# Kernel tuning notes

Measured on AMD Instinct MI355X. Metric: run time of the kernel, lower is better.

Reference implementation:

```python
import jax, jax.numpy as jnp
import numpy as np

VOCAB, POS = 50000, 64
WDIM, PDIM = 256, 64
LSTM_H = 512          # total bidirectional width
H = LSTM_H // 2       # per-direction hidden
MLP = 512
SEQ = 512


def _lstm_dir(x, Wih, Whh, bih, bhh, reverse):
    # x: [T, in]; Wih: [4H, in]; Whh: [4H, H]; gate order i,f,g,o (PyTorch)
    Hd = Whh.shape[1]
    def step(carry, xt):
        h, c = carry
        g = xt @ Wih.T + bih + h @ Whh.T + bhh
        i, f, gg, o = jnp.split(g, 4, axis=-1)
        c = jax.nn.sigmoid(f) * c + jax.nn.sigmoid(i) * jnp.tanh(gg)
        h = jax.nn.sigmoid(o) * jnp.tanh(c)
        return (h, c), h
    xs = x[::-1] if reverse else x
    init = (jnp.zeros((Hd,), x.dtype), jnp.zeros((Hd,), x.dtype))
    _, hs = jax.lax.scan(step, init, xs)
    return hs[::-1] if reverse else hs


def _bilstm_layer(x, Wih, Whh, bih, bhh):
    # params stacked over direction: [2, ...]
    hf = _lstm_dir(x, Wih[0], Whh[0], bih[0], bhh[0], False)
    hb = _lstm_dir(x, Wih[1], Whh[1], bih[1], bhh[1], True)
    return jnp.concatenate([hf, hb], axis=-1)  # [T, 2H]


def setup_inputs() -> dict:
    key = jax.random.key(0)
    ks = jax.random.split(key, 16)
    s = 0.05
    inp = {
        "word_tensor": jax.random.randint(ks[0], (SEQ,), 0, VOCAB),
        "pos_tensor": jax.random.randint(ks[1], (SEQ,), 0, POS),
        "word_emb": jax.random.normal(ks[2], (VOCAB, WDIM), jnp.float32) * s,
        "pos_emb": jax.random.normal(ks[3], (POS, PDIM), jnp.float32) * s,
        # layer 0: input = WDIM+PDIM = 320
        "wih0": jax.random.normal(ks[4], (2, 4 * H, WDIM + PDIM), jnp.float32) * s,
        "whh0": jax.random.normal(ks[5], (2, 4 * H, H), jnp.float32) * s,
        "bih0": jax.random.normal(ks[6], (2, 4 * H), jnp.float32) * s,
        "bhh0": jax.random.normal(ks[7], (2, 4 * H), jnp.float32) * s,
        # layer 1: input = 2H = LSTM_H
        "wih1": jax.random.normal(ks[8], (2, 4 * H, LSTM_H), jnp.float32) * s,
        "whh1": jax.random.normal(ks[9], (2, 4 * H, H), jnp.float32) * s,
        "bih1": jax.random.normal(ks[10], (2, 4 * H), jnp.float32) * s,
        "bhh1": jax.random.normal(ks[11], (2, 4 * H), jnp.float32) * s,
        # pairwise MLP: Linear(2*LSTM_H -> MLP), output_layer(MLP -> 1)
        "W_lin": jax.random.normal(ks[12], (MLP, 2 * LSTM_H), jnp.float32) * s,
        "b_lin": jax.random.normal(ks[13], (MLP,), jnp.float32) * s,
        "w_out": jax.random.normal(ks[14], (1, MLP), jnp.float32) * s,
        "b_out": jax.random.normal(ks[15], (1,), jnp.float32) * s,
    }
    return inp


def reference(word_tensor, pos_tensor, word_emb, pos_emb,
              wih0, whh0, bih0, bhh0, wih1, whh1, bih1, bhh1,
              W_lin, b_lin, w_out, b_out):
    # embeddings: [T, 320]
    embeds = jnp.concatenate([word_emb[word_tensor], pos_emb[pos_tensor]], axis=-1)
    x = _bilstm_layer(embeds, wih0, whh0, bih0, bhh0)
    lstm_out = _bilstm_layer(x, wih1, whh1, bih1, bhh1)  # [T, LSTM_H]
    # Fused pairwise scoring: Linear(cat(h_h, h_m)) = h_h @ W1.T + h_m @ W2.T + b
    W1, W2 = W_lin[:, :LSTM_H], W_lin[:, LSTM_H:]
    u = lstm_out @ W1.T  # [T, MLP] head half
    v = lstm_out @ W2.T  # [T, MLP] modifier half
    neuron = jnp.tanh(u[:, None, :] + v[None, :, :] + b_lin)  # [T, T, MLP]
    score = neuron @ w_out[0] + b_out[0]                      # [T, T]
    n = score.shape[0]
    # original puts NaN on the diagonal (invalid h==m pairs); use 0.0 sentinel
    return jnp.where(jnp.eye(n, dtype=bool), 0.0, score)
```

## Files before the change

kernel.cpp:

```cpp
#include <hip/hip_runtime.h>
#include <cstddef>
#include <cstdint>

constexpr int kSeq = 512;
constexpr int kH   = 256;
constexpr int kG   = 1024;
constexpr int kE   = 320;
constexpr int kLH  = 512;
constexpr int kMLP = 512;

typedef _Float16 h2 __attribute__((ext_vector_type(2)));

__device__ __forceinline__ float fexp2f(float x) {
  float r; asm("v_exp_f32 %0, %1" : "=v"(r) : "v"(x)); return r;
}
__device__ __forceinline__ float frcpf(float x) {
  float r; asm("v_rcp_f32 %0, %1" : "=v"(r) : "v"(x)); return r;
}
__device__ __forceinline__ float sigm(float x) {
  return frcpf(1.0f + fexp2f(-1.4426950408889634f * x));
}
__device__ __forceinline__ float tanh_(float x) {
  return 1.0f - 2.0f * frcpf(1.0f + fexp2f(2.8853900817779268f * x));
}

__device__ __forceinline__ float fdot2(unsigned int w, unsigned int h, float c) {
#if __has_builtin(__builtin_amdgcn_fdot2)
  return __builtin_amdgcn_fdot2(__builtin_bit_cast(h2, w),
                                __builtin_bit_cast(h2, h), c, false);
#else
  const h2 wv = __builtin_bit_cast(h2, w);
  const h2 hv = __builtin_bit_cast(h2, h);
  return c + (float)wv.x * (float)hv.x + (float)wv.y * (float)hv.y;
#endif
}

__device__ __forceinline__ unsigned int packh2(float a, float b) {
  h2 v; v.x = (_Float16)a; v.y = (_Float16)b;
  return __builtin_bit_cast(unsigned int, v);
}

__global__ void embed_k(const int* __restrict__ wt, const int* __restrict__ pt,
                        const float* __restrict__ we, const float* __restrict__ pe,
                        float* __restrict__ X) {
  const int t = blockIdx.x;
  const int c = threadIdx.x;
  const int w = wt[t];
  const int p = pt[t];
  X[t * kE + c] = (c < 256) ? we[(size_t)w * 256 + c] : pe[p * 64 + (c - 256)];
}

__global__ __launch_bounds__(256) void pack_wh_k(
    const float* __restrict__ whh0, const float* __restrict__ whh1,
    unsigned int* __restrict__ wh16) {
  const int idx = blockIdx.x * 256 + threadIdx.x;
  const int layer = idx >> 18;
  const int li = idx & 262143;
  const int rowg = li >> 7;
  const int c2 = li & 127;
  const float* src = (layer ? whh1 : whh0) + (size_t)rowg * kH + c2 * 2;
  wh16[idx] = packh2(src[0], src[1]);
}

template <int BM, int BN, int BK>
__global__ __launch_bounds__(256) void gemm_nt(
    const float* __restrict__ A, int lda,
    const float* __restrict__ B, int ldb,
    const float* __restrict__ b1, const float* __restrict__ b2, float scale,
    float* __restrict__ C, int csm, int csn, int K) {
  const int tid = threadIdx.x;
  const int m0 = blockIdx.y * BM;
  const int n0 = blockIdx.x * BN;
  __shared__ float As[BK][BM];
  __shared__ float Bs[BK][BN];
  const int lm = tid >> 2;
  const int lk = tid & 3;
  const int tx = tid & 15;
  const int ty = tid >> 4;
  float acc[4][4] = {};
  for (int k0 = 0; k0 < K; k0 += BK) {
    const float4 av = *(const float4*)(A + (size_t)(m0 + lm) * lda + k0 + lk * 4);
    const float4 bv = *(const float4*)(B + (size_t)(n0 + lm) * ldb + k0 + lk * 4);
    __syncthreads();
    As[lk * 4 + 0][lm] = av.x; As[lk * 4 + 1][lm] = av.y;
    As[lk * 4 + 2][lm] = av.z; As[lk * 4 + 3][lm] = av.w;
    Bs[lk * 4 + 0][lm] = bv.x; Bs[lk * 4 + 1][lm] = bv.y;
    Bs[lk * 4 + 2][lm] = bv.z; Bs[lk * 4 + 3][lm] = bv.w;
    __syncthreads();
#pragma unroll
    for (int kk = 0; kk < BK; ++kk) {
      const float4 a = *(const float4*)&As[kk][ty * 4];
      const float4 b = *(const float4*)&Bs[kk][tx * 4];
      acc[0][0] = fmaf(a.x, b.x, acc[0][0]);
      acc[0][1] = fmaf(a.x, b.y, acc[0][1]);
      acc[0][2] = fmaf(a.x, b.z, acc[0][2]);
      acc[0][3] = fmaf(a.x, b.w, acc[0][3]);
      acc[1][0] = fmaf(a.y, b.x, acc[1][0]);
      acc[1][1] = fmaf(a.y, b.y, acc[1][1]);
      acc[1][2] = fmaf(a.y, b.z, acc[1][2]);
      acc[1][3] = fmaf(a.y, b.w, acc[1][3]);
      acc[2][0] = fmaf(a.z, b.x, acc[2][0]);
      acc[2][1] = fmaf(a.z, b.y, acc[2][1]);
      acc[2][2] = fmaf(a.z, b.z, acc[2][2]);
      acc[2][3] = fmaf(a.z, b.w, acc[2][3]);
      acc[3][0] = fmaf(a.w, b.x, acc[3][0]);
      acc[3][1] = fmaf(a.w, b.y, acc[3][1]);
      acc[3][2] = fmaf(a.w, b.z, acc[3][2]);
      acc[3][3] = fmaf(a.w, b.w, acc[3][3]);
    }
  }
#pragma unroll
  for (int ii = 0; ii < 4; ++ii) {
#pragma unroll
    for (int jj = 0; jj < 4; ++jj) {
      const int m = m0 + ty * 4 + ii;
      const int n = n0 + tx * 4 + jj;
      float v = acc[ii][jj];
      if (b1) v += b1[n];
      if (b2) v += b2[n];
      C[(size_t)m * csm + (size_t)n * csn] = v * scale;
    }
  }
}

__global__ __launch_bounds__(1024)
__attribute__((amdgpu_waves_per_eu(4, 4)))
void lstm_scan_2cu(
    const unsigned int* __restrict__ wh16,
    const float* __restrict__ pre,
    float* __restrict__ out,
    float* __restrict__ comm)
{
  const int d = blockIdx.x >> 1;
  const int s = blockIdx.x & 1;
  const int t = threadIdx.x;
  const int w = t >> 6;
  const int L = t & 63;
  const int ch = w & 1;
  const int r  = (w >> 1) * 64 + L;
  const int g  = r >> 7;
  const int j  = r & 127;
  const int grow = g * kH + s * 128 + j;
  const bool early = (ch == s);

  uint4 wr[16];
  {
    const uint4* wp = (const uint4*)wh16 + ((size_t)d * kG + grow) * 32 + ch * 16;
#pragma unroll
    for (int k = 0; k < 16; ++k) wr[k] = wp[k];
  }

  __shared__ __align__(16) _Float16 hh16[kH];
  __shared__ float pbuf[512];
  __shared__ float gbuf[512];
  if (t < 128) ((h2*)hh16)[t] = h2{(_Float16)0.f, (_Float16)0.f};
  float c = 0.0f;
  __syncthreads();

  const uint4* hh4 = (const uint4*)hh16;
  float* cm = comm + (size_t)d * kSeq * kH;

  const bool isPoller = early && ((w >> 1) < 2);
  const int pe = (w >> 1) * 64 + L;
  const int re = (1 - s) * 128 + pe;

  for (int u = 0; u < kSeq; ++u) {
    const int ts = d ? (kSeq - 1 - u) : u;
    float pg = 0.0f;
    if (!early) pg = pre[((size_t)d * kSeq + ts) * kG + grow];

    if (early) {
      const uint4* hp = hh4 + ch * 16;
      float a0 = 0.f, a1 = 0.f, a2 = 0.f, a3 = 0.f;
#pragma unroll
      for (int k = 0; k < 16; ++k) {
        const uint4 hv = hp[k];
        a0 = fdot2(wr[k].x, hv.x, a0);
        a1 = fdot2(wr[k].y, hv.y, a1);
        a2 = fdot2(wr[k].z, hv.z, a2);
        a3 = fdot2(wr[k].w, hv.w, a3);
      }
      pbuf[r] = (a0 + a1) + (a2 + a3);
      if (isPoller && u > 0) {
        const float* src = &cm[(size_t)(u - 1) * kH + re];
        float a = __hip_atomic_load(src, __ATOMIC_RELAXED, __HIP_MEMORY_SCOPE_AGENT);
        float b = __hip_atomic_load(src, __ATOMIC_RELAXED, __HIP_MEMORY_SCOPE_AGENT);
        while (a == 0.0f) {
          a = b;
          b = __hip_atomic_load(src, __ATOMIC_RELAXED, __HIP_MEMORY_SCOPE_AGENT);
        }
        hh16[re] = (_Float16)(a - 2.0f);
      }
    }
    __syncthreads();

    if (!early) {
      const uint4* hp = hh4 + ch * 16;
      float a0 = 0.f, a1 = 0.f, a2 = 0.f, a3 = 0.f;
#pragma unroll
      for (int k = 0; k < 16; ++k) {
        const uint4 hv = hp[k];
        a0 = fdot2(wr[k].x, hv.x, a0);
        a1 = fdot2(wr[k].y, hv.y, a1);
        a2 = fdot2(wr[k].z, hv.z, a2);
        a3 = fdot2(wr[k].w, hv.w, a3);
      }
      gbuf[r] = pbuf[r] + (a0 + a1) + (a2 + a3) + pg;
    }
    __syncthreads();

    if (t < 128) {
      const float gi = gbuf[t];
      const float gf = gbuf[128 + t];
      const float gg = gbuf[256 + t];
      const float go = gbuf[384 + t];
      const float iv = sigm(gi), fv = sigm(gf);
      const float gv = tanh_(gg), ov = sigm(go);
      c = fv * c + iv * gv;
      const float h = ov * tanh_(c);
      const int e = s * 128 + t;
      __hip_atomic_store(&cm[(size_t)u * kH + e], h + 2.0f,
                         __ATOMIC_RELAXED, __HIP_MEMORY_SCOPE_AGENT);
      hh16[e] = (_Float16)h;
      out[(size_t)ts * kLH + d * kH + e] = h;
    }
    __syncthreads();
  }
}

__global__ __launch_bounds__(512) void score_k(
    const float* __restrict__ Up, const float* __restrict__ VT,
    const float* __restrict__ wout, const float* __restrict__ bout,
    float* __restrict__ out) {
  const int i = blockIdx.x;
  const int j = threadIdx.x;
  __shared__ float u_sh[kMLP];
  __shared__ float w_sh[kMLP];
  u_sh[j] = Up[(size_t)i * kMLP + j];
  w_sh[j] = wout[j];
  __syncthreads();
  float acc = 0.0f;
#pragma unroll 4
  for (int m = 0; m < kMLP; ++m) {
    const float x = u_sh[m] + VT[(size_t)m * kSeq + j];
    const float th = 1.0f - 2.0f * frcpf(1.0f + fexp2f(x));
    acc = fmaf(th, w_sh[m], acc);
  }
  const float s = acc + bout[0];
  out[(size_t)i * kSeq + j] = (j == i) ? 0.0f : s;
}

extern "C" void kernel_launch(void* const* d_in, const int* in_sizes, int n_in,
                              void* d_out, int out_size, void* d_ws, size_t ws_size,
                              hipStream_t stream) {
  const int*   wt   = (const int*)d_in[0];
  const int*   pt   = (const int*)d_in[1];
  const float* wemb = (const float*)d_in[2];
  const float* pemb = (const float*)d_in[3];
  const float* wih0 = (const float*)d_in[4];
  const float* whh0 = (const float*)d_in[5];
  const float* bih0 = (const float*)d_in[6];
  const float* bhh0 = (const float*)d_in[7];
  const float* wih1 = (const float*)d_in[8];
  const float* whh1 = (const float*)d_in[9];
  const float* bih1 = (const float*)d_in[10];
  const float* bhh1 = (const float*)d_in[11];
  const float* wlin = (const float*)d_in[12];
  const float* blin = (const float*)d_in[13];
  const float* wout = (const float*)d_in[14];
  const float* bout = (const float*)d_in[15];
  float* outp = (float*)d_out;

  float* ws   = (float*)d_ws;
  float* X    = ws;
  float* PG0  = X + kSeq * kE;
  float* X1   = PG0 + 2 * kSeq * kG;
  float* PG1  = X1 + kSeq * kLH;
  float* LOUT = PG1 + 2 * kSeq * kG;
  float* U    = LOUT + kSeq * kLH;
  float* VT   = U + kSeq * kMLP;
  float* COMM0 = VT + kSeq * kMLP;
  float* COMM1 = COMM0 + 2 * kSeq * kH;
  unsigned int* WH16 = (unsigned int*)(COMM1 + 2 * kSeq * kH);

  const float SC = 2.8853900817779268f;

  hipMemsetAsync(COMM0, 0, 2 * 2 * kSeq * kH * sizeof(float), stream);

  embed_k<<<kSeq, kE, 0, stream>>>(wt, pt, wemb, pemb, X);
  pack_wh_k<<<2048, 256, 0, stream>>>(whh0, whh1, WH16);

  for (int d = 0; d < 2; ++d) {
    gemm_nt<64, 64, 16><<<dim3(kG / 64, kSeq / 64), 256, 0, stream>>>(
        X, kE, wih0 + (size_t)d * kG * kE, kE,
        bih0 + d * kG, bhh0 + d * kG, 1.0f,
        PG0 + (size_t)d * kSeq * kG, kG, 1, kE);
  }
  lstm_scan_2cu<<<4, 1024, 0, stream>>>(WH16, PG0, X1, COMM0);

  for (int d = 0; d < 2; ++d) {
    gemm_nt<64, 64, 16><<<dim3(kG / 64, kSeq / 64), 256, 0, stream>>>(
        X1, kLH, wih1 + (size_t)d * kG * kLH, kLH,
        bih1 + d * kG, bhh1 + d * kG, 1.0f,
        PG1 + (size_t)d * kSeq * kG, kG, 1, kLH);
  }
  lstm_scan_2cu<<<4, 1024, 0, stream>>>(WH16 + 2 * kG * 128, PG1, LOUT, COMM1);

  gemm_nt<64, 64, 16><<<dim3(kMLP / 64, kSeq / 64), 256, 0, stream>>>(
      LOUT, kLH, wlin, 2 * kLH, nullptr, nullptr, SC,
      U, kMLP, 1, kLH);
  gemm_nt<64, 64, 16><<<dim3(kMLP / 64, kSeq / 64), 256, 0, stream>>>(
      LOUT, kLH, wlin + kLH, 2 * kLH, blin, nullptr, SC,
      VT, 1, kSeq, kLH);

  score_k<<<kSeq, 512, 0, stream>>>(U, VT, wout, bout, outp);
}
```

Measured before the change: 1.940 ms.

## Restructure 2-CU LSTM step to two barriers with dedicated poller wave

Before, each recurrent step ran an early half-dot product that overlapped with polling for the peer CU's h, then a late half, then the gate stage, separated by three barriers. Now both halves of the dot product run together into a double pbuf. Gate threads add the partial sums plus the preactivation loads, and a separate group of waves polls the peer's h for the current step in the same phase. This drops one barrier per step. The cost is that the peer-h wait now sits on the critical path just before the next step's barrier, rather than overlapping with half of the matvec.

```diff
diff --git a/kernel.cpp b/kernel.cpp
--- a/kernel.cpp
+++ b/kernel.cpp
@@ -141,7 +141,6 @@
   const int g  = r >> 7;
   const int j  = r & 127;
   const int grow = g * kH + s * 128 + j;
-  const bool early = (ch == s);
 
   uint4 wr[16];
   {
@@ -151,25 +150,25 @@
   }
 
   __shared__ __align__(16) _Float16 hh16[kH];
-  __shared__ float pbuf[512];
-  __shared__ float gbuf[512];
+  __shared__ float pbuf[2][512];
   if (t < 128) ((h2*)hh16)[t] = h2{(_Float16)0.f, (_Float16)0.f};
   float c = 0.0f;
   __syncthreads();
 
   const uint4* hh4 = (const uint4*)hh16;
   float* cm = comm + (size_t)d * kSeq * kH;
-
-  const bool isPoller = early && ((w >> 1) < 2);
-  const int pe = (w >> 1) * 64 + L;
-  const int re = (1 - s) * 128 + pe;
+  const bool isGate = (t < 128);
+  const bool isPoll = (t >= 512 && t < 640);
+  const int re = (1 - s) * 128 + (t - 512);
 
   for (int u = 0; u < kSeq; ++u) {
     const int ts = d ? (kSeq - 1 - u) : u;
-    float pg = 0.0f;
-    if (!early) pg = pre[((size_t)d * kSeq + ts) * kG + grow];
-
-    if (early) {
+    float pg0 = 0.f, pg1 = 0.f, pg2 = 0.f, pg3 = 0.f;
+    if (isGate) {
+      const float* pp = pre + ((size_t)d * kSeq + ts) * kG + s * 128 + t;
+      pg0 = pp[0]; pg1 = pp[256]; pg2 = pp[512]; pg3 = pp[768];
+    }
+    {
       const uint4* hp = hh4 + ch * 16;
       float a0 = 0.f, a1 = 0.f, a2 = 0.f, a3 = 0.f;
 #pragma unroll
@@ -180,40 +179,15 @@
         a2 = fdot2(wr[k].z, hv.z, a2);
         a3 = fdot2(wr[k].w, hv.w, a3);
       }
-      pbuf[r] = (a0 + a1) + (a2 + a3);
-      if (isPoller && u > 0) {
-        const float* src = &cm[(size_t)(u - 1) * kH + re];
-        float a = __hip_atomic_load(src, __ATOMIC_RELAXED, __HIP_MEMORY_SCOPE_AGENT);
-        float b = __hip_atomic_load(src, __ATOMIC_RELAXED, __HIP_MEMORY_SCOPE_AGENT);
-        while (a == 0.0f) {
-          a = b;
-          b = __hip_atomic_load(src, __ATOMIC_RELAXED, __HIP_MEMORY_SCOPE_AGENT);
-        }
-        hh16[re] = (_Float16)(a - 2.0f);
-      }
+      pbuf[ch][r] = (a0 + a1) + (a2 + a3);
     }
     __syncthreads();
 
-    if (!early) {
-      const uint4* hp = hh4 + ch * 16;
-      float a0 = 0.f, a1 = 0.f, a2 = 0.f, a3 = 0.f;
-#pragma unroll
-      for (int k = 0; k < 16; ++k) {
-        const uint4 hv = hp[k];
-        a0 = fdot2(wr[k].x, hv.x, a0);
-        a1 = fdot2(wr[k].y, hv.y, a1);
-        a2 = fdot2(wr[k].z, hv.z, a2);
-        a3 = fdot2(wr[k].w, hv.w, a3);
-      }
-      gbuf[r] = pbuf[r] + (a0 + a1) + (a2 + a3) + pg;
-    }
-    __syncthreads();
-
-    if (t < 128) {
-      const float gi = gbuf[t];
-      const float gf = gbuf[128 + t];
-      const float gg = gbuf[256 + t];
-      const float go = gbuf[384 + t];
+    if (isGate) {
+      const float gi = pbuf[0][t]       + pbuf[1][t]       + pg0;
+      const float gf = pbuf[0][128 + t] + pbuf[1][128 + t] + pg1;
+      const float gg = pbuf[0][256 + t] + pbuf[1][256 + t] + pg2;
+      const float go = pbuf[0][384 + t] + pbuf[1][384 + t] + pg3;
       const float iv = sigm(gi), fv = sigm(gf);
       const float gv = tanh_(gg), ov = sigm(go);
       c = fv * c + iv * gv;
@@ -223,6 +197,15 @@
                          __ATOMIC_RELAXED, __HIP_MEMORY_SCOPE_AGENT);
       hh16[e] = (_Float16)h;
       out[(size_t)ts * kLH + d * kH + e] = h;
+    } else if (isPoll) {
+      const float* src = &cm[(size_t)u * kH + re];
+      float a = __hip_atomic_load(src, __ATOMIC_RELAXED, __HIP_MEMORY_SCOPE_AGENT);
+      float b = __hip_atomic_load(src, __ATOMIC_RELAXED, __HIP_MEMORY_SCOPE_AGENT);
+      while (a == 0.0f) {
+        a = b;
+        b = __hip_atomic_load(src, __ATOMIC_RELAXED, __HIP_MEMORY_SCOPE_AGENT);
+      }
+      hh16[re] = (_Float16)(a - 2.0f);
     }
     __syncthreads();
   }
```

New measurement: 1.721 ms. -11.3%, faster.
